# Performance work log

Measured on AMD Instinct MI355X. Metric: run time of the kernel, lower is better.

Reference implementation:

```python
import jax, jax.numpy as jnp
import numpy as np

BN_EPS = 1e-5
NN_CHUNK = 1024  # unknown points processed per distance-matrix tile


def _batch_ids(cnt, total):
    # contiguous per-batch layout -> batch id of each point via cumsum/searchsorted
    return jnp.searchsorted(jnp.cumsum(cnt), jnp.arange(total), side='right')


def three_nn(unknown, known, ub_id, kb_id):
    """Ragged brute-force 3-NN. Returns (squared dists [N,3], global idx [N,3])."""
    N = unknown.shape[0]
    nchunk = N // NN_CHUNK
    u = unknown.reshape(nchunk, NN_CHUNK, 3)
    ub = ub_id.reshape(nchunk, NN_CHUNK)

    def body(args):
        uc, bc = args
        d2 = jnp.sum((uc[:, None, :] - known[None, :, :]) ** 2, axis=-1)  # [chunk, M]
        d2 = jnp.where(bc[:, None] == kb_id[None, :], d2, jnp.inf)  # mask cross-batch pairs
        neg_d, idx = jax.lax.top_k(-d2, 3)
        return -neg_d, idx

    d2, idx = jax.lax.map(body, (u, ub))
    return d2.reshape(N, 3), idx.reshape(N, 3)


def three_interpolate(known_feats, idx, weight):
    # gather [N,3,C] then inverse-distance weighted sum -> [N,C]
    gathered = known_feats[idx]  # [N,3,C]
    return jnp.einsum('nkc,nk->nc', gathered, weight)


def conv_bn_relu(x, W, gamma, beta):
    # 1x1 Conv2d over [1,C,N,1] == pointwise matmul; BN (training stats) over points
    h = x @ W.T  # [N, C_out]
    mean = jnp.mean(h, axis=0)
    var = jnp.mean((h - mean) ** 2, axis=0)  # biased, as torch BN normalization
    h = (h - mean) * jax.lax.rsqrt(var + BN_EPS) * gamma + beta
    return jax.nn.relu(h)


def setup_inputs() -> dict:
    key = jax.random.key(0)
    ks = jax.random.split(key, 10)
    B, Nper, Mper, C1, C2 = 4, 16384, 4096, 128, 256
    N, M = B * Nper, B * Mper
    unknown = jax.random.normal(ks[0], (N, 3), jnp.float32) * 10.0
    known = jax.random.normal(ks[1], (M, 3), jnp.float32) * 10.0
    unknown_feats = jax.random.normal(ks[2], (N, C1), jnp.float32)
    known_feats = jax.random.normal(ks[3], (M, C2), jnp.float32)
    unknown_batch_cnt = jnp.full((B,), Nper, jnp.int32)
    known_batch_cnt = jnp.full((B,), Mper, jnp.int32)
    Cin = C1 + C2  # 384
    W1 = jax.random.normal(ks[4], (256, Cin), jnp.float32) * (1.0 / np.sqrt(Cin))
    W2 = jax.random.normal(ks[5], (256, 256), jnp.float32) * (1.0 / np.sqrt(256))
    g1 = jnp.ones((256,), jnp.float32); b1 = jnp.zeros((256,), jnp.float32)
    g2 = jnp.ones((256,), jnp.float32); b2 = jnp.zeros((256,), jnp.float32)
    return {"unknown": unknown, "unknown_batch_cnt": unknown_batch_cnt,
            "known": known, "known_batch_cnt": known_batch_cnt,
            "unknown_feats": unknown_feats, "known_feats": known_feats,
            "W1": W1, "g1": g1, "b1": b1, "W2": W2, "g2": g2, "b2": b2}


def reference(unknown, unknown_batch_cnt, known, known_batch_cnt,
              unknown_feats, known_feats, W1, g1, b1, W2, g2, b2):
    ub_id = _batch_ids(unknown_batch_cnt, unknown.shape[0])
    kb_id = _batch_ids(known_batch_cnt, known.shape[0])
    dist, idx = three_nn(unknown, known, ub_id, kb_id)  # squared dists, as CUDA kernel
    dist_recip = 1.0 / (dist + 1e-8)
    weight = dist_recip / jnp.sum(dist_recip, axis=-1, keepdims=True)
    interpolated = three_interpolate(known_feats, idx, weight)  # [N, C2]
    new_features = jnp.concatenate([interpolated, unknown_feats], axis=1)  # [N, C2+C1]
    new_features = conv_bn_relu(new_features, W1, g1, b1)
    new_features = conv_bn_relu(new_features, W2, g2, b2)
    return new_features  # [N, 256]
```

## Files before the change

### kernel.cpp

```cpp
#include <hip/hip_runtime.h>
#include <math.h>

typedef __attribute__((ext_vector_type(8))) short short8;
typedef __attribute__((ext_vector_type(4))) float f32x4;

#define INF 3.0e38f
#define BN_EPS 1e-5f

#define NB 1024
#define XMIN (-64.0f)
#define BW 0.125f
#define INVW 8.0f

__device__ __forceinline__ unsigned short f2bf(float x) {
    union { float f; unsigned u; } v; v.f = x;
    unsigned r = v.u + 0x7FFF + ((v.u >> 16) & 1);
    return (unsigned short)(r >> 16);
}
__device__ __forceinline__ float bf2f(unsigned short u) {
    return __uint_as_float(((unsigned)u) << 16);
}

__global__ __launch_bounds__(256) void hist2_kernel(
    const float* __restrict__ kn, const int* __restrict__ kcnt, int M,
    const float* __restrict__ un, const int* __restrict__ ucnt, int N,
    int B, int* __restrict__ kc, int* __restrict__ qc)
{
    int j = blockIdx.x * 256 + threadIdx.x;
    const float* P; const int* C; int* out; int idx;
    if (j < M) { P = kn; C = kcnt; out = kc; idx = j; }
    else { idx = j - M; if (idx >= N) return; P = un; C = ucnt; out = qc; }
    int cum = 0, bb = 0;
    for (int i = 0; i < B; i++) { int c = C[i]; if (idx >= cum) bb = i; cum += c; }
    float x = P[idx * 3];
    int bi = (int)((x - XMIN) * INVW);
    bi = min(max(bi, 0), NB - 1);
    atomicAdd(&out[bb * NB + bi], 1);
}

__global__ __launch_bounds__(1024) void scan2_kernel(
    const int* __restrict__ kc, int* __restrict__ kbs, int* __restrict__ kcur,
    const int* __restrict__ qc, int* __restrict__ qbs, int* __restrict__ qcur,
    int T)
{
    __shared__ int ts[1024];
    const int* cnt = blockIdx.x ? qc : kc;
    int* bs  = blockIdx.x ? qbs : kbs;
    int* cur = blockIdx.x ? qcur : kcur;

    int tid = threadIdx.x;
    int base = tid * 4;
    int v0 = 0, v1 = 0, v2 = 0, v3 = 0;
    if (base + 0 < T) v0 = cnt[base + 0];
    if (base + 1 < T) v1 = cnt[base + 1];
    if (base + 2 < T) v2 = cnt[base + 2];
    if (base + 3 < T) v3 = cnt[base + 3];
    int s = v0 + v1 + v2 + v3;
    ts[tid] = s;
    __syncthreads();
    for (int off = 1; off < 1024; off <<= 1) {
        int t = (tid >= off) ? ts[tid - off] : 0;
        __syncthreads();
        ts[tid] += t;
        __syncthreads();
    }
    int ex = ts[tid] - s;
    if (base + 0 < T) { bs[base + 0] = ex; cur[base + 0] = ex; } ex += v0;
    if (base + 1 < T) { bs[base + 1] = ex; cur[base + 1] = ex; } ex += v1;
    if (base + 2 < T) { bs[base + 2] = ex; cur[base + 2] = ex; } ex += v2;
    if (base + 3 < T) { bs[base + 3] = ex; cur[base + 3] = ex; } ex += v3;
    if (tid == ((T - 1) >> 2)) bs[T] = ts[tid];
}

__global__ __launch_bounds__(256) void scatter2_kernel(
    const float* __restrict__ kn, const int* __restrict__ kcnt, int M,
    const float* __restrict__ un, const int* __restrict__ ucnt, int N,
    int B, int* __restrict__ kcur, float4* __restrict__ kscat,
    int* __restrict__ qcur, float4* __restrict__ qscat)
{
    int j = blockIdx.x * 256 + threadIdx.x;
    const float* P; const int* C; int* cur; float4* out; int idx;
    if (j < M) { P = kn; C = kcnt; cur = kcur; out = kscat; idx = j; }
    else { idx = j - M; if (idx >= N) return; P = un; C = ucnt; cur = qcur; out = qscat; }
    int cum = 0, bb = 0;
    for (int i = 0; i < B; i++) { int c = C[i]; if (idx >= cum) bb = i; cum += c; }
    float x = P[idx * 3], y = P[idx * 3 + 1], z = P[idx * 3 + 2];
    int bi = (int)((x - XMIN) * INVW);
    bi = min(max(bi, 0), NB - 1);
    int pos = atomicAdd(&cur[bb * NB + bi], 1);
    out[pos] = make_float4(x, y, z, __int_as_float(idx));
}

__global__ __launch_bounds__(256) void knn3_grid2_kernel(
    const int* __restrict__ ucnt, const int* __restrict__ kbs,
    const float4* __restrict__ qscat, const float4* __restrict__ scat,
    int B, float* __restrict__ wgt, int* __restrict__ idxo)
{
    __shared__ float md[4][64][3];
    __shared__ unsigned long long mk[64][4][3];

    int tid = threadIdx.x;
    int wv = tid >> 6;
    int lane = tid & 63;
    int pbase = blockIdx.x * 64;
    int qpos = pbase + lane;

    int cum = 0, bb = 0;
    for (int i = 0; i < B; i++) { int c = ucnt[i]; if (pbase >= cum) bb = i; cum += c; }

    float4 qf = qscat[qpos];
    float ux = qf.x, uy = qf.y, uz = qf.z;

    int kst = kbs[bb * NB];
    int ken = kbs[bb * NB + NB];

    int bq = (int)((ux - XMIN) * INVW);
    bq = min(max(bq, 0), NB - 1);
    int sp = kbs[bb * NB + bq];
    int lo = sp - 16;
    if (lo < kst) lo = kst;
    if (lo + 32 > ken) lo = ken - 32;
    if (lo < kst) lo = kst;

    float d0 = INF, d1 = INF, d2v = INF;
    int alo = lo + wv * 8;
    int ahi = min(alo + 8, ken);
    for (int c = alo; c < ahi; c++) {
        float4 f = scat[c];
        float dx = f.x - ux, dy = f.y - uy, dz = f.z - uz;
        float e = __builtin_fmaf(dx, dx, __builtin_fmaf(dy, dy, dz * dz));
        float m0 = fmaxf(e, d0), m1 = fmaxf(e, d1);
        d0 = fminf(e, d0); d1 = fminf(m0, d1); d2v = fminf(m1, d2v);
    }
    md[wv][lane][0] = d0; md[wv][lane][1] = d1; md[wv][lane][2] = d2v;
    __syncthreads();

    d0 = INF; d1 = INF; d2v = INF;
#pragma unroll
    for (int w = 0; w < 4; w++)
#pragma unroll
        for (int k = 0; k < 3; k++) {
            float e = md[w][lane][k];
            float m0 = fmaxf(e, d0), m1 = fmaxf(e, d1);
            d0 = fminf(e, d0); d1 = fminf(m0, d1); d2v = fminf(m1, d2v);
        }
    float thr = d2v;

    float W = fminf(sqrtf(thr), 300.0f);
    int blo = max((int)((ux - W - XMIN) * INVW) - 1, 0);
    int bhi = min((int)((ux + W - XMIN) * INVW) + 1, NB - 1);
    int pLo = kbs[bb * NB + blo];
    int pHi = kbs[bb * NB + bhi + 1];

    int wlo = pLo, whi = pHi;
#pragma unroll
    for (int s = 1; s < 64; s <<= 1) {
        wlo = min(wlo, __shfl_xor(wlo, s, 64));
        whi = max(whi, __shfl_xor(whi, s, 64));
    }

    int chunks = (whi - wlo + 7) >> 3;
    int cpw = (chunks + 3) >> 2;
    int c0 = min(wv * cpw, chunks);
    int c1 = min(c0 + cpw, chunks);
    int mylo = wlo + (c0 << 3);
    int myhi = min(wlo + (c1 << 3), whi);
    mylo = __builtin_amdgcn_readfirstlane(mylo);
    myhi = __builtin_amdgcn_readfirstlane(myhi);

    unsigned long long k0 = ~0ULL, k1 = ~0ULL, k2 = ~0ULL;
    auto insK = [&](unsigned long long k) {
        bool cc0 = k < k0;
        unsigned long long t0 = cc0 ? k : k0;
        unsigned long long t1 = cc0 ? k0 : k;
        bool cc1 = t1 < k1;
        unsigned long long u0 = cc1 ? t1 : k1;
        unsigned long long u1 = cc1 ? k1 : t1;
        k0 = t0; k1 = u0;
        k2 = u1 < k2 ? u1 : k2;
    };

    const float4* kq = scat + mylo;
    int n = myhi - mylo;
    int nf = n & ~7;
    for (int i = 0; i < nf; i += 8) {
        float ex[8]; int ix[8];
#pragma unroll
        for (int c = 0; c < 8; c++) {
            float4 f = kq[i + c];
            float dx = f.x - ux, dy = f.y - uy, dz = f.z - uz;
            ex[c] = __builtin_fmaf(dx, dx, __builtin_fmaf(dy, dy, dz * dz));
            ix[c] = __float_as_int(f.w);
        }
        float m8 = fminf(fminf(fminf(ex[0], ex[1]), fminf(ex[2], ex[3])),
                         fminf(fminf(ex[4], ex[5]), fminf(ex[6], ex[7])));
        if (m8 <= thr) {
#pragma unroll
            for (int c = 0; c < 8; c++) {
                if (ex[c] <= thr) {
                    insK(((unsigned long long)__float_as_uint(ex[c]) << 32) |
                         (unsigned)ix[c]);
                    thr = fminf(thr, __uint_as_float((unsigned)(k2 >> 32)));
                }
            }
        }
    }
    for (int i = nf; i < n; i++) {
        float4 f = kq[i];
        float dx = f.x - ux, dy = f.y - uy, dz = f.z - uz;
        float e = __builtin_fmaf(dx, dx, __builtin_fmaf(dy, dy, dz * dz));
        if (e <= thr) {
            insK(((unsigned long long)__float_as_uint(e) << 32) |
                 (unsigned)__float_as_int(f.w));
            thr = fminf(thr, __uint_as_float((unsigned)(k2 >> 32)));
        }
    }

    mk[lane][wv][0] = k0; mk[lane][wv][1] = k1; mk[lane][wv][2] = k2;
    __syncthreads();

    if (tid < 64) {
        unsigned long long a0 = ~0ULL, a1 = ~0ULL, a2 = ~0ULL;
        auto ins2 = [&](unsigned long long k) {
            bool cc0 = k < a0;
            unsigned long long t0 = cc0 ? k : a0;
            unsigned long long t1 = cc0 ? a0 : k;
            bool cc1 = t1 < a1;
            unsigned long long u0 = cc1 ? t1 : a1;
            unsigned long long u1 = cc1 ? a1 : t1;
            a0 = t0; a1 = u0;
            a2 = u1 < a2 ? u1 : a2;
        };
#pragma unroll
        for (int r = 0; r < 4; r++)
#pragma unroll
            for (int kk = 0; kk < 3; kk++)
                ins2(mk[tid][r][kk]);

        float dd0 = __uint_as_float((unsigned)(a0 >> 32));
        float dd1 = __uint_as_float((unsigned)(a1 >> 32));
        float dd2 = __uint_as_float((unsigned)(a2 >> 32));
        float r0 = 1.0f / (dd0 + 1e-8f);
        float r1 = 1.0f / (dd1 + 1e-8f);
        float r2 = 1.0f / (dd2 + 1e-8f);
        float rs = 1.0f / (r0 + r1 + r2);
        int orig = __float_as_int(qscat[pbase + tid].w);
        wgt[orig * 3 + 0] = r0 * rs;
        wgt[orig * 3 + 1] = r1 * rs;
        wgt[orig * 3 + 2] = r2 * rs;
        idxo[orig * 3 + 0] = (int)(unsigned)a0;
        idxo[orig * 3 + 1] = (int)(unsigned)a1;
        idxo[orig * 3 + 2] = (int)(unsigned)a2;
    }
}

__global__ __launch_bounds__(256) void wconv_kernel(
    const float* __restrict__ W1, const float* __restrict__ W2,
    unsigned short* __restrict__ W1b, unsigned short* __restrict__ W2b,
    int n1, int n2)
{
    int i = blockIdx.x * 256 + threadIdx.x;
    if (i < n1) W1b[i] = f2bf(W1[i]);
    int j = i - n1;
    if (j >= 0 && j < n2) W2b[j] = f2bf(W2[j]);
}

template <int K, int MODE>
__global__ __launch_bounds__(256) void gemm_bf16_kernel(
    const void* __restrict__ Aa, const float* __restrict__ ufeat,
    const unsigned short* __restrict__ W,
    const float* __restrict__ wgt, const int* __restrict__ idxv,
    const float* __restrict__ bnsum, const float* __restrict__ bnsq,
    const float* __restrict__ bng, const float* __restrict__ bnb, float invN,
    void* __restrict__ Cv, float* __restrict__ gsum, float* __restrict__ gsq)
{
    __shared__ unsigned short As[128 * 40];
    __shared__ unsigned short Bs[128 * 40];
    __shared__ float colsum[128];
    __shared__ float colsq[128];
    __shared__ float sc[256], sh[256];

    int tid = threadIdx.x;
    int w = tid >> 6, lane = tid & 63;
    int r = w >> 1, cq = w & 1;
    int m16 = lane & 15, q = lane >> 4;
    int bm = blockIdx.x * 128, bn = blockIdx.y * 128;

    if (MODE == 1) {
        float mean = bnsum[tid] * invN;
        float var = bnsq[tid] * invN - mean * mean;
        float scv = bng[tid] * rsqrtf(var + BN_EPS);
        sc[tid] = scv;
        sh[tid] = bnb[tid] - mean * scv;
    }

    int srow = tid >> 2;
    int kc = (tid & 3) * 8;
    float w0a[2], w1a[2], w2a[2];
    int j0a[2], j1a[2], j2a[2];
    if (MODE == 2) {
#pragma unroll
        for (int t = 0; t < 2; t++) {
            int pp = bm + srow + 64 * t;
            w0a[t] = wgt[pp * 3 + 0]; w1a[t] = wgt[pp * 3 + 1]; w2a[t] = wgt[pp * 3 + 2];
            j0a[t] = idxv[pp * 3 + 0]; j1a[t] = idxv[pp * 3 + 1]; j2a[t] = idxv[pp * 3 + 2];
        }
    }

    f32x4 acc[4][4];
#pragma unroll
    for (int i = 0; i < 4; i++)
#pragma unroll
        for (int j = 0; j < 4; j++) acc[i][j] = (f32x4){0.f, 0.f, 0.f, 0.f};

#pragma unroll
    for (int k0 = 0; k0 < K; k0 += 32) {
        __syncthreads();
#pragma unroll
        for (int t = 0; t < 2; t++) {
            int row = srow + 64 * t;
            int c = k0 + kc;
            ushort4 o0, o1;
            if (MODE == 2) {
                if (c < 256) {
                    const float* f0 = (const float*)Aa + (size_t)j0a[t] * 256 + c;
                    const float* f1 = (const float*)Aa + (size_t)j1a[t] * 256 + c;
                    const float* f2 = (const float*)Aa + (size_t)j2a[t] * 256 + c;
                    float4 x0 = *(const float4*)f0, x1 = *(const float4*)(f0 + 4);
                    float4 y0 = *(const float4*)f1, y1 = *(const float4*)(f1 + 4);
                    float4 z0 = *(const float4*)f2, z1 = *(const float4*)(f2 + 4);
                    float W0 = w0a[t], W1 = w1a[t], W2 = w2a[t];
                    o0.x = f2bf(x0.x * W0 + y0.x * W1 + z0.x * W2);
                    o0.y = f2bf(x0.y * W0 + y0.y * W1 + z0.y * W2);
                    o0.z = f2bf(x0.z * W0 + y0.z * W1 + z0.z * W2);
                    o0.w = f2bf(x0.w * W0 + y0.w * W1 + z0.w * W2);
                    o1.x = f2bf(x1.x * W0 + y1.x * W1 + z1.x * W2);
                    o1.y = f2bf(x1.y * W0 + y1.y * W1 + z1.y * W2);
                    o1.z = f2bf(x1.z * W0 + y1.z * W1 + z1.z * W2);
                    o1.w = f2bf(x1.w * W0 + y1.w * W1 + z1.w * W2);
                } else {
                    const float* fu = ufeat + (size_t)(bm + row) * 128 + (c - 256);
                    float4 u0 = *(const float4*)fu, u1 = *(const float4*)(fu + 4);
                    o0.x = f2bf(u0.x); o0.y = f2bf(u0.y);
                    o0.z = f2bf(u0.z); o0.w = f2bf(u0.w);
                    o1.x = f2bf(u1.x); o1.y = f2bf(u1.y);
                    o1.z = f2bf(u1.z); o1.w = f2bf(u1.w);
                }
            } else {
                const unsigned short* Ab = (const unsigned short*)Aa;
                ushort4 h0 = *(const ushort4*)(Ab + (size_t)(bm + row) * K + c);
                ushort4 h1v = *(const ushort4*)(Ab + (size_t)(bm + row) * K + c + 4);
                float4 s0 = *(const float4*)&sc[c];
                float4 s1 = *(const float4*)&sc[c + 4];
                float4 t0 = *(const float4*)&sh[c];
                float4 t1 = *(const float4*)&sh[c + 4];
                o0.x = f2bf(fmaxf(bf2f(h0.x) * s0.x + t0.x, 0.f));
                o0.y = f2bf(fmaxf(bf2f(h0.y) * s0.y + t0.y, 0.f));
                o0.z = f2bf(fmaxf(bf2f(h0.z) * s0.z + t0.z, 0.f));
                o0.w = f2bf(fmaxf(bf2f(h0.w) * s0.w + t0.w, 0.f));
                o1.x = f2bf(fmaxf(bf2f(h1v.x) * s1.x + t1.x, 0.f));
                o1.y = f2bf(fmaxf(bf2f(h1v.y) * s1.y + t1.y, 0.f));
                o1.z = f2bf(fmaxf(bf2f(h1v.z) * s1.z + t1.z, 0.f));
                o1.w = f2bf(fmaxf(bf2f(h1v.w) * s1.w + t1.w, 0.f));
            }
            *(ushort4*)&As[row * 40 + kc] = o0;
            *(ushort4*)&As[row * 40 + kc + 4] = o1;
            *(short8*)&Bs[row * 40 + kc] =
                *(const short8*)(W + (size_t)(bn + row) * K + k0 + kc);
        }
        __syncthreads();

        short8 af[4], bf[4];
#pragma unroll
        for (int sub = 0; sub < 4; sub++) {
            af[sub] = *(const short8*)&As[(r * 64 + sub * 16 + m16) * 40 + q * 8];
            bf[sub] = *(const short8*)&Bs[(cq * 64 + sub * 16 + m16) * 40 + q * 8];
        }
#pragma unroll
        for (int sm = 0; sm < 4; sm++)
#pragma unroll
            for (int sn = 0; sn < 4; sn++)
                acc[sm][sn] = __builtin_amdgcn_mfma_f32_16x16x32_bf16(
                    af[sm], bf[sn], acc[sm][sn], 0, 0, 0);
    }

    int row0 = bm + r * 64 + q * 4;
    int col0 = bn + cq * 64 + m16;
#pragma unroll
    for (int sm = 0; sm < 4; sm++)
#pragma unroll
        for (int sn = 0; sn < 4; sn++) {
            f32x4 v = acc[sm][sn];
#pragma unroll
            for (int reg = 0; reg < 4; reg++) {
                size_t idx = (size_t)(row0 + sm * 16 + reg) * 256 + col0 + sn * 16;
                if (MODE == 2) ((unsigned short*)Cv)[idx] = f2bf(v[reg]);
                else           ((float*)Cv)[idx] = v[reg];
            }
        }

    __syncthreads();
    if (tid < 128) { colsum[tid] = 0.f; colsq[tid] = 0.f; }
    __syncthreads();
#pragma unroll
    for (int sn = 0; sn < 4; sn++) {
        float sacc = 0.f, qacc = 0.f;
#pragma unroll
        for (int sm = 0; sm < 4; sm++) {
            f32x4 v = acc[sm][sn];
#pragma unroll
            for (int reg = 0; reg < 4; reg++) {
                sacc += v[reg];
                qacc += v[reg] * v[reg];
            }
        }
        int lc = cq * 64 + sn * 16 + m16;
        atomicAdd(&colsum[lc], sacc);
        atomicAdd(&colsq[lc], qacc);
    }
    __syncthreads();
    if (tid < 128) {
        atomicAdd(&gsum[bn + tid], colsum[tid]);
        atomicAdd(&gsq[bn + tid], colsq[tid]);
    }
}

__global__ __launch_bounds__(256) void final_act_kernel(
    const float* __restrict__ h2, const float* __restrict__ bnsum,
    const float* __restrict__ bnsq, const float* __restrict__ bng,
    const float* __restrict__ bnb, float invN,
    float* __restrict__ out, int total4)
{
    __shared__ float sc[256], sh[256];
    int c = threadIdx.x;
    float mean = bnsum[c] * invN;
    float var = bnsq[c] * invN - mean * mean;
    float scv = bng[c] * rsqrtf(var + BN_EPS);
    sc[c] = scv;
    sh[c] = bnb[c] - mean * scv;
    __syncthreads();

    int i = blockIdx.x * 256 + threadIdx.x;
    if (i >= total4) return;
    int c4 = i & 63;
    float4 v = ((const float4*)h2)[i];
    float4 s = *(const float4*)&sc[c4 * 4];
    float4 t = *(const float4*)&sh[c4 * 4];
    float4 o;
    o.x = fmaxf(v.x * s.x + t.x, 0.0f);
    o.y = fmaxf(v.y * s.y + t.y, 0.0f);
    o.z = fmaxf(v.z * s.z + t.z, 0.0f);
    o.w = fmaxf(v.w * s.w + t.w, 0.0f);
    ((float4*)out)[i] = o;
}

extern "C" void kernel_launch(void* const* d_in, const int* in_sizes, int n_in,
                              void* d_out, int out_size, void* d_ws, size_t ws_size,
                              hipStream_t stream)
{
    const float* unknown = (const float*)d_in[0];
    const int*   ucnt    = (const int*)d_in[1];
    const float* known   = (const float*)d_in[2];
    const int*   kcnt    = (const int*)d_in[3];
    const float* ufeat   = (const float*)d_in[4];
    const float* kfeat   = (const float*)d_in[5];
    const float* W1      = (const float*)d_in[6];
    const float* g1      = (const float*)d_in[7];
    const float* b1      = (const float*)d_in[8];
    const float* W2      = (const float*)d_in[9];
    const float* g2      = (const float*)d_in[10];
    const float* b2      = (const float*)d_in[11];

    int N = in_sizes[0] / 3;
    int B = in_sizes[1];
    int M = in_sizes[2] / 3;
    int T = B * NB;

    char* ws = (char*)d_ws;
    size_t off = 0;
    float* wgt = (float*)(ws + off);            off += (size_t)N * 3 * 4;
    int*   idxb = (int*)(ws + off);             off += (size_t)N * 3 * 4;
    float* stats = (float*)(ws + off);          off += 4 * 256 * 4;
    float* sum1 = stats,        *sq1 = stats + 256;
    float* sum2 = stats + 512,  *sq2 = stats + 768;
    int* kch = (int*)(ws + off);                off += (size_t)T * 4;
    int* qch = (int*)(ws + off);                off += (size_t)T * 4;
    int* kbs = (int*)(ws + off);                off += ((size_t)T + 1) * 4;
    int* qbs = (int*)(ws + off);                off += ((size_t)T + 1) * 4;
    int* kcur = (int*)(ws + off);               off += (size_t)T * 4;
    int* qcur = (int*)(ws + off);               off += (size_t)T * 4;
    unsigned short* W1b = (unsigned short*)(ws + off);  off += 256 * 384 * 2;
    unsigned short* W2b = (unsigned short*)(ws + off);  off += 256 * 256 * 2;
    off = (off + 255) & ~(size_t)255;
    float4* kscat = (float4*)(ws + off);        off += (size_t)M * sizeof(float4);
    float4* qscat = (float4*)(ws + off);        off += (size_t)N * sizeof(float4);
    off = (off + 255) & ~(size_t)255;
    unsigned short* h1 = (unsigned short*)(ws + off);   off += (size_t)N * 256 * 2;
    off = (off + 255) & ~(size_t)255;
    float* h2 = (float*)(ws + off);

    float invN = 1.0f / (float)N;

    hipMemsetAsync(stats, 0, 4 * 256 * 4 + 2 * (size_t)T * 4, stream);

    wconv_kernel<<<(256 * 384 + 256 * 256 + 255) / 256, 256, 0, stream>>>(
        W1, W2, W1b, W2b, 256 * 384, 256 * 256);

    hist2_kernel<<<(M + N + 255) / 256, 256, 0, stream>>>(
        known, kcnt, M, unknown, ucnt, N, B, kch, qch);
    scan2_kernel<<<2, 1024, 0, stream>>>(kch, kbs, kcur, qch, qbs, qcur, T);
    scatter2_kernel<<<(M + N + 255) / 256, 256, 0, stream>>>(
        known, kcnt, M, unknown, ucnt, N, B, kcur, kscat, qcur, qscat);
    knn3_grid2_kernel<<<N / 64, 256, 0, stream>>>(ucnt, kbs, qscat, kscat,
                                                  B, wgt, idxb);

    gemm_bf16_kernel<384, 2><<<dim3(N / 128, 2), 256, 0, stream>>>(
        kfeat, ufeat, W1b, wgt, idxb,
        nullptr, nullptr, nullptr, nullptr, 0.f, h1, sum1, sq1);
    gemm_bf16_kernel<256, 1><<<dim3(N / 128, 2), 256, 0, stream>>>(
        h1, nullptr, W2b, nullptr, nullptr,
        sum1, sq1, g1, b1, invN, h2, sum2, sq2);
    final_act_kernel<<<N / 4, 256, 0, stream>>>(h2, sum2, sq2, g2, b2, invN,
                                                (float*)d_out, N * 64);
}
```

Baseline: 406.2 us.

## Widen KNN seed window to wave-uniform 256 points and drop threshold-gated insertion

The first-pass seed search now starts from one wave-uniform base and covers 256 sorted candidates split across four waves, instead of 32 per-lane candidates. The goal is a tighter initial distance threshold, which shrinks the slab of x-bins scanned in the second pass. The second pass drops the per-candidate threshold test and branch, and inserts every candidate branch-free with a 4-wide unroll. This trades extra seed-phase loads and unconditional 64-bit insert work for less divergence and a smaller scan window. Because the seed window is anchored on lane 0's bin, seeds for other lanes in the wave may be poorer.

After: 443.0 us. 1.09x slower.

```diff
diff --git a/kernel.cpp b/kernel.cpp
--- a/kernel.cpp
+++ b/kernel.cpp
@@ -11,6 +11,7 @@
 #define XMIN (-64.0f)
 #define BW 0.125f
 #define INVW 8.0f
+#define PHA 256
 
 __device__ __forceinline__ unsigned short f2bf(float x) {
     union { float f; unsigned u; } v; v.f = x;
@@ -91,7 +92,7 @@
     out[pos] = make_float4(x, y, z, __int_as_float(idx));
 }
 
-__global__ __launch_bounds__(256) void knn3_grid2_kernel(
+__global__ __launch_bounds__(256) void knn3_grid3_kernel(
     const int* __restrict__ ucnt, const int* __restrict__ kbs,
     const float4* __restrict__ qscat, const float4* __restrict__ scat,
     int B, float* __restrict__ wgt, int* __restrict__ idxo)
@@ -103,12 +104,11 @@
     int wv = tid >> 6;
     int lane = tid & 63;
     int pbase = blockIdx.x * 64;
-    int qpos = pbase + lane;
 
     int cum = 0, bb = 0;
     for (int i = 0; i < B; i++) { int c = ucnt[i]; if (pbase >= cum) bb = i; cum += c; }
 
-    float4 qf = qscat[qpos];
+    float4 qf = qscat[pbase + lane];
     float ux = qf.x, uy = qf.y, uz = qf.z;
 
     int kst = kbs[bb * NB];
@@ -117,20 +117,36 @@
     int bq = (int)((ux - XMIN) * INVW);
     bq = min(max(bq, 0), NB - 1);
     int sp = kbs[bb * NB + bq];
-    int lo = sp - 16;
-    if (lo < kst) lo = kst;
-    if (lo + 32 > ken) lo = ken - 32;
-    if (lo < kst) lo = kst;
+    int sp0 = __builtin_amdgcn_readfirstlane(sp);
+    int abase = sp0 - (PHA / 2);
+    if (abase + PHA > ken) abase = ken - PHA;
+    if (abase < kst) abase = kst;
+
+    int alo = abase + wv * (PHA / 4);
+    int ahi = min(alo + (PHA / 4), ken);
 
     float d0 = INF, d1 = INF, d2v = INF;
-    int alo = lo + wv * 8;
-    int ahi = min(alo + 8, ken);
-    for (int c = alo; c < ahi; c++) {
-        float4 f = scat[c];
-        float dx = f.x - ux, dy = f.y - uy, dz = f.z - uz;
-        float e = __builtin_fmaf(dx, dx, __builtin_fmaf(dy, dy, dz * dz));
-        float m0 = fmaxf(e, d0), m1 = fmaxf(e, d1);
-        d0 = fminf(e, d0); d1 = fminf(m0, d1); d2v = fminf(m1, d2v);
+    {
+        const float4* ka = scat + alo;
+        int na = ahi - alo;
+        int i = 0;
+        for (; i + 4 <= na; i += 4) {
+#pragma unroll
+            for (int c = 0; c < 4; c++) {
+                float4 f = ka[i + c];
+                float dx = f.x - ux, dy = f.y - uy, dz = f.z - uz;
+                float e = __builtin_fmaf(dx, dx, __builtin_fmaf(dy, dy, dz * dz));
+                float m0 = fmaxf(e, d0), m1 = fmaxf(e, d1);
+                d0 = fminf(e, d0); d1 = fminf(m0, d1); d2v = fminf(m1, d2v);
+            }
+        }
+        for (; i < na; i++) {
+            float4 f = ka[i];
+            float dx = f.x - ux, dy = f.y - uy, dz = f.z - uz;
+            float e = __builtin_fmaf(dx, dx, __builtin_fmaf(dy, dy, dz * dz));
+            float m0 = fmaxf(e, d0), m1 = fmaxf(e, d1);
+            d0 = fminf(e, d0); d1 = fminf(m0, d1); d2v = fminf(m1, d2v);
+        }
     }
     md[wv][lane][0] = d0; md[wv][lane][1] = d1; md[wv][lane][2] = d2v;
     __syncthreads();
@@ -159,12 +175,12 @@
         whi = max(whi, __shfl_xor(whi, s, 64));
     }
 
-    int chunks = (whi - wlo + 7) >> 3;
+    int chunks = (whi - wlo + 3) >> 2;
     int cpw = (chunks + 3) >> 2;
     int c0 = min(wv * cpw, chunks);
     int c1 = min(c0 + cpw, chunks);
-    int mylo = wlo + (c0 << 3);
-    int myhi = min(wlo + (c1 << 3), whi);
+    int mylo = wlo + (c0 << 2);
+    int myhi = min(wlo + (c1 << 2), whi);
     mylo = __builtin_amdgcn_readfirstlane(mylo);
     myhi = __builtin_amdgcn_readfirstlane(myhi);
 
@@ -182,38 +198,23 @@
 
     const float4* kq = scat + mylo;
     int n = myhi - mylo;
-    int nf = n & ~7;
-    for (int i = 0; i < nf; i += 8) {
-        float ex[8]; int ix[8];
-#pragma unroll
-        for (int c = 0; c < 8; c++) {
+    int i = 0;
+    for (; i + 4 <= n; i += 4) {
+#pragma unroll
+        for (int c = 0; c < 4; c++) {
             float4 f = kq[i + c];
             float dx = f.x - ux, dy = f.y - uy, dz = f.z - uz;
-            ex[c] = __builtin_fmaf(dx, dx, __builtin_fmaf(dy, dy, dz * dz));
-            ix[c] = __float_as_int(f.w);
-        }
-        float m8 = fminf(fminf(fminf(ex[0], ex[1]), fminf(ex[2], ex[3])),
-                         fminf(fminf(ex[4], ex[5]), fminf(ex[6], ex[7])));
-        if (m8 <= thr) {
-#pragma unroll
-            for (int c = 0; c < 8; c++) {
-                if (ex[c] <= thr) {
-                    insK(((unsigned long long)__float_as_uint(ex[c]) << 32) |
-                         (unsigned)ix[c]);
-                    thr = fminf(thr, __uint_as_float((unsigned)(k2 >> 32)));
-                }
-            }
-        }
-    }
-    for (int i = nf; i < n; i++) {
+            float e = __builtin_fmaf(dx, dx, __builtin_fmaf(dy, dy, dz * dz));
+            insK(((unsigned long long)__float_as_uint(e) << 32) |
+                 (unsigned)__float_as_int(f.w));
+        }
+    }
+    for (; i < n; i++) {
         float4 f = kq[i];
         float dx = f.x - ux, dy = f.y - uy, dz = f.z - uz;
         float e = __builtin_fmaf(dx, dx, __builtin_fmaf(dy, dy, dz * dz));
-        if (e <= thr) {
-            insK(((unsigned long long)__float_as_uint(e) << 32) |
-                 (unsigned)__float_as_int(f.w));
-            thr = fminf(thr, __uint_as_float((unsigned)(k2 >> 32)));
-        }
+        insK(((unsigned long long)__float_as_uint(e) << 32) |
+             (unsigned)__float_as_int(f.w));
     }
 
     mk[lane][wv][0] = k0; mk[lane][wv][1] = k1; mk[lane][wv][2] = k2;
@@ -511,7 +512,7 @@
     scan2_kernel<<<2, 1024, 0, stream>>>(kch, kbs, kcur, qch, qbs, qcur, T);
     scatter2_kernel<<<(M + N + 255) / 256, 256, 0, stream>>>(
         known, kcnt, M, unknown, ucnt, N, B, kcur, kscat, qcur, qscat);
-    knn3_grid2_kernel<<<N / 64, 256, 0, stream>>>(ucnt, kbs, qscat, kscat,
+    knn3_grid3_kernel<<<N / 64, 256, 0, stream>>>(ucnt, kbs, qscat, kscat,
                                                   B, wgt, idxb);
 
     gemm_bf16_kernel<384, 2><<<dim3(N / 128, 2), 256, 0, stream>>>(
```

## Split each KNN query across 4 lanes with shuffle-based merges

Applied to the files above, without the earlier changes.

Reworks the 3-NN search so each wave handles 16 queries, with 4 lanes per query splitting the candidate range, instead of one lane per query across 4 waves. The initial threshold window grows from 32 to 192 points, which should tighten the pruning bound. Cross-lane top-3 merges now use wave shuffles, which removes the shared-memory staging and the block syncs. Each query now scans only its own x-slab rather than the union over 64 queries. The larger seed window costs more work per query, and divergence among the 16 queries in a wave may differ.

Measured after the change: 416.6 us. 2.6% more time.

```diff
diff --git a/kernel.cpp b/kernel.cpp
--- a/kernel.cpp
+++ b/kernel.cpp
@@ -11,6 +11,7 @@
 #define XMIN (-64.0f)
 #define BW 0.125f
 #define INVW 8.0f
+#define PA 192
 
 __device__ __forceinline__ unsigned short f2bf(float x) {
     union { float f; unsigned u; } v; v.f = x;
@@ -19,6 +20,11 @@
 }
 __device__ __forceinline__ float bf2f(unsigned short u) {
     return __uint_as_float(((unsigned)u) << 16);
+}
+__device__ __forceinline__ unsigned long long shflx_u64(unsigned long long v, int m) {
+    int lo = __shfl_xor((int)(unsigned)(v & 0xFFFFFFFFULL), m, 64);
+    int hi = __shfl_xor((int)(unsigned)(v >> 32), m, 64);
+    return ((unsigned long long)(unsigned)hi << 32) | (unsigned)lo;
 }
 
 __global__ __launch_bounds__(256) void hist2_kernel(
@@ -91,19 +97,18 @@
     out[pos] = make_float4(x, y, z, __int_as_float(idx));
 }
 
-__global__ __launch_bounds__(256) void knn3_grid2_kernel(
+__global__ __launch_bounds__(256) void knn4_kernel(
     const int* __restrict__ ucnt, const int* __restrict__ kbs,
     const float4* __restrict__ qscat, const float4* __restrict__ scat,
     int B, float* __restrict__ wgt, int* __restrict__ idxo)
 {
-    __shared__ float md[4][64][3];
-    __shared__ unsigned long long mk[64][4][3];
-
     int tid = threadIdx.x;
     int wv = tid >> 6;
     int lane = tid & 63;
+    int qi = lane & 15;
+    int r4 = lane >> 4;
     int pbase = blockIdx.x * 64;
-    int qpos = pbase + lane;
+    int qpos = pbase + wv * 16 + qi;
 
     int cum = 0, bb = 0;
     for (int i = 0; i < B; i++) { int c = ucnt[i]; if (pbase >= cum) bb = i; cum += c; }
@@ -117,56 +122,56 @@
     int bq = (int)((ux - XMIN) * INVW);
     bq = min(max(bq, 0), NB - 1);
     int sp = kbs[bb * NB + bq];
-    int lo = sp - 16;
-    if (lo < kst) lo = kst;
-    if (lo + 32 > ken) lo = ken - 32;
-    if (lo < kst) lo = kst;
+
+    int abase = sp - PA / 2;
+    if (abase + PA > ken) abase = ken - PA;
+    if (abase < kst) abase = kst;
+    int aend = min(abase + PA, ken);
 
     float d0 = INF, d1 = INF, d2v = INF;
-    int alo = lo + wv * 8;
-    int ahi = min(alo + 8, ken);
-    for (int c = alo; c < ahi; c++) {
-        float4 f = scat[c];
-        float dx = f.x - ux, dy = f.y - uy, dz = f.z - uz;
-        float e = __builtin_fmaf(dx, dx, __builtin_fmaf(dy, dy, dz * dz));
+    auto upd = [&](float e) {
         float m0 = fmaxf(e, d0), m1 = fmaxf(e, d1);
         d0 = fminf(e, d0); d1 = fminf(m0, d1); d2v = fminf(m1, d2v);
-    }
-    md[wv][lane][0] = d0; md[wv][lane][1] = d1; md[wv][lane][2] = d2v;
-    __syncthreads();
-
-    d0 = INF; d1 = INF; d2v = INF;
-#pragma unroll
-    for (int w = 0; w < 4; w++)
-#pragma unroll
-        for (int k = 0; k < 3; k++) {
-            float e = md[w][lane][k];
-            float m0 = fmaxf(e, d0), m1 = fmaxf(e, d1);
-            d0 = fminf(e, d0); d1 = fminf(m0, d1); d2v = fminf(m1, d2v);
-        }
+    };
+    {
+        int alo = abase + r4 * (PA / 4);
+        int ahi = min(alo + PA / 4, aend);
+        int i = alo;
+        for (; i + 4 <= ahi; i += 4) {
+            float e[4];
+#pragma unroll
+            for (int c = 0; c < 4; c++) {
+                float4 f = scat[i + c];
+                float dx = f.x - ux, dy = f.y - uy, dz = f.z - uz;
+                e[c] = __builtin_fmaf(dx, dx, __builtin_fmaf(dy, dy, dz * dz));
+            }
+#pragma unroll
+            for (int c = 0; c < 4; c++) upd(e[c]);
+        }
+        for (; i < ahi; i++) {
+            float4 f = scat[i];
+            float dx = f.x - ux, dy = f.y - uy, dz = f.z - uz;
+            upd(__builtin_fmaf(dx, dx, __builtin_fmaf(dy, dy, dz * dz)));
+        }
+    }
+#pragma unroll
+    for (int s = 16; s <= 32; s <<= 1) {
+        float e0 = __shfl_xor(d0, s, 64);
+        float e1 = __shfl_xor(d1, s, 64);
+        float e2 = __shfl_xor(d2v, s, 64);
+        upd(e0); upd(e1); upd(e2);
+    }
     float thr = d2v;
 
-    float W = fminf(sqrtf(thr), 300.0f);
-    int blo = max((int)((ux - W - XMIN) * INVW) - 1, 0);
-    int bhi = min((int)((ux + W - XMIN) * INVW) + 1, NB - 1);
+    float Wr = fminf(sqrtf(thr), 300.0f);
+    int blo = max((int)((ux - Wr - XMIN) * INVW) - 1, 0);
+    int bhi = min((int)((ux + Wr - XMIN) * INVW) + 1, NB - 1);
     int pLo = kbs[bb * NB + blo];
     int pHi = kbs[bb * NB + bhi + 1];
-
-    int wlo = pLo, whi = pHi;
-#pragma unroll
-    for (int s = 1; s < 64; s <<= 1) {
-        wlo = min(wlo, __shfl_xor(wlo, s, 64));
-        whi = max(whi, __shfl_xor(whi, s, 64));
-    }
-
-    int chunks = (whi - wlo + 7) >> 3;
-    int cpw = (chunks + 3) >> 2;
-    int c0 = min(wv * cpw, chunks);
-    int c1 = min(c0 + cpw, chunks);
-    int mylo = wlo + (c0 << 3);
-    int myhi = min(wlo + (c1 << 3), whi);
-    mylo = __builtin_amdgcn_readfirstlane(mylo);
-    myhi = __builtin_amdgcn_readfirstlane(myhi);
+    int n = pHi - pLo;
+    int quar = (n + 3) >> 2;
+    int mylo = pLo + r4 * quar;
+    int myhi = min(mylo + quar, pHi);
 
     unsigned long long k0 = ~0ULL, k1 = ~0ULL, k2 = ~0ULL;
     auto insK = [&](unsigned long long k) {
@@ -180,33 +185,30 @@
         k2 = u1 < k2 ? u1 : k2;
     };
 
-    const float4* kq = scat + mylo;
-    int n = myhi - mylo;
-    int nf = n & ~7;
-    for (int i = 0; i < nf; i += 8) {
-        float ex[8]; int ix[8];
-#pragma unroll
-        for (int c = 0; c < 8; c++) {
-            float4 f = kq[i + c];
+    int i = mylo;
+    for (; i + 4 <= myhi; i += 4) {
+        float e[4]; int ix[4];
+#pragma unroll
+        for (int c = 0; c < 4; c++) {
+            float4 f = scat[i + c];
             float dx = f.x - ux, dy = f.y - uy, dz = f.z - uz;
-            ex[c] = __builtin_fmaf(dx, dx, __builtin_fmaf(dy, dy, dz * dz));
+            e[c] = __builtin_fmaf(dx, dx, __builtin_fmaf(dy, dy, dz * dz));
             ix[c] = __float_as_int(f.w);
         }
-        float m8 = fminf(fminf(fminf(ex[0], ex[1]), fminf(ex[2], ex[3])),
-                         fminf(fminf(ex[4], ex[5]), fminf(ex[6], ex[7])));
-        if (m8 <= thr) {
-#pragma unroll
-            for (int c = 0; c < 8; c++) {
-                if (ex[c] <= thr) {
-                    insK(((unsigned long long)__float_as_uint(ex[c]) << 32) |
+        float m4 = fminf(fminf(e[0], e[1]), fminf(e[2], e[3]));
+        if (m4 <= thr) {
+#pragma unroll
+            for (int c = 0; c < 4; c++) {
+                if (e[c] <= thr) {
+                    insK(((unsigned long long)__float_as_uint(e[c]) << 32) |
                          (unsigned)ix[c]);
                     thr = fminf(thr, __uint_as_float((unsigned)(k2 >> 32)));
                 }
             }
         }
     }
-    for (int i = nf; i < n; i++) {
-        float4 f = kq[i];
+    for (; i < myhi; i++) {
+        float4 f = scat[i];
         float dx = f.x - ux, dy = f.y - uy, dz = f.z - uz;
         float e = __builtin_fmaf(dx, dx, __builtin_fmaf(dy, dy, dz * dz));
         if (e <= thr) {
@@ -216,41 +218,29 @@
         }
     }
 
-    mk[lane][wv][0] = k0; mk[lane][wv][1] = k1; mk[lane][wv][2] = k2;
-    __syncthreads();
-
-    if (tid < 64) {
-        unsigned long long a0 = ~0ULL, a1 = ~0ULL, a2 = ~0ULL;
-        auto ins2 = [&](unsigned long long k) {
-            bool cc0 = k < a0;
-            unsigned long long t0 = cc0 ? k : a0;
-            unsigned long long t1 = cc0 ? a0 : k;
-            bool cc1 = t1 < a1;
-            unsigned long long u0 = cc1 ? t1 : a1;
-            unsigned long long u1 = cc1 ? a1 : t1;
-            a0 = t0; a1 = u0;
-            a2 = u1 < a2 ? u1 : a2;
-        };
-#pragma unroll
-        for (int r = 0; r < 4; r++)
-#pragma unroll
-            for (int kk = 0; kk < 3; kk++)
-                ins2(mk[tid][r][kk]);
-
-        float dd0 = __uint_as_float((unsigned)(a0 >> 32));
-        float dd1 = __uint_as_float((unsigned)(a1 >> 32));
-        float dd2 = __uint_as_float((unsigned)(a2 >> 32));
+#pragma unroll
+    for (int s = 16; s <= 32; s <<= 1) {
+        unsigned long long e0 = shflx_u64(k0, s);
+        unsigned long long e1 = shflx_u64(k1, s);
+        unsigned long long e2 = shflx_u64(k2, s);
+        insK(e0); insK(e1); insK(e2);
+    }
+
+    if (r4 == 0) {
+        float dd0 = __uint_as_float((unsigned)(k0 >> 32));
+        float dd1 = __uint_as_float((unsigned)(k1 >> 32));
+        float dd2 = __uint_as_float((unsigned)(k2 >> 32));
         float r0 = 1.0f / (dd0 + 1e-8f);
         float r1 = 1.0f / (dd1 + 1e-8f);
         float r2 = 1.0f / (dd2 + 1e-8f);
         float rs = 1.0f / (r0 + r1 + r2);
-        int orig = __float_as_int(qscat[pbase + tid].w);
+        int orig = __float_as_int(qf.w);
         wgt[orig * 3 + 0] = r0 * rs;
         wgt[orig * 3 + 1] = r1 * rs;
         wgt[orig * 3 + 2] = r2 * rs;
-        idxo[orig * 3 + 0] = (int)(unsigned)a0;
-        idxo[orig * 3 + 1] = (int)(unsigned)a1;
-        idxo[orig * 3 + 2] = (int)(unsigned)a2;
+        idxo[orig * 3 + 0] = (int)(unsigned)k0;
+        idxo[orig * 3 + 1] = (int)(unsigned)k1;
+        idxo[orig * 3 + 2] = (int)(unsigned)k2;
     }
 }
 
@@ -511,8 +501,8 @@
     scan2_kernel<<<2, 1024, 0, stream>>>(kch, kbs, kcur, qch, qbs, qcur, T);
     scatter2_kernel<<<(M + N + 255) / 256, 256, 0, stream>>>(
         known, kcnt, M, unknown, ucnt, N, B, kcur, kscat, qcur, qscat);
-    knn3_grid2_kernel<<<N / 64, 256, 0, stream>>>(ucnt, kbs, qscat, kscat,
-                                                  B, wgt, idxb);
+    knn4_kernel<<<N / 64, 256, 0, stream>>>(ucnt, kbs, qscat, kscat,
+                                            B, wgt, idxb);
 
     gemm_bf16_kernel<384, 2><<<dim3(N / 128, 2), 256, 0, stream>>>(
         kfeat, ufeat, W1b, wgt, idxb,
```
